# Optimization experiments

Measured on AMD Instinct MI355X. Metric: run time of the kernel, lower is better.

Reference implementation:

```python
import jax, jax.numpy as jnp
import numpy as np

D = 1024
H = 16
HD = D // H
EPS = 1e-5


def layer_norm(x, g, b):
    mu = jnp.mean(x, axis=-1, keepdims=True)
    var = jnp.var(x, axis=-1, keepdims=True)
    return (x - mu) * jax.lax.rsqrt(var + EPS) * g + b


def setup_inputs() -> dict:
    key = jax.random.key(0)
    ks = jax.random.split(key, 16)
    s = 0.02
    return {
        "x": jax.random.normal(ks[0], (2, 2048, D), jnp.float32),
        "ln1_g": jnp.ones((D,), jnp.float32),
        "ln1_b": jnp.zeros((D,), jnp.float32),
        "Wq": jax.random.normal(ks[1], (D, D), jnp.float32) * s,
        "bq": jnp.zeros((D,), jnp.float32),
        "Wk": jax.random.normal(ks[2], (D, D), jnp.float32) * s,
        "bk": jnp.zeros((D,), jnp.float32),
        "Wv": jax.random.normal(ks[3], (D, D), jnp.float32) * s,
        "bv": jnp.zeros((D,), jnp.float32),
        "Wo": jax.random.normal(ks[4], (D, D), jnp.float32) * s,
        "bo": jnp.zeros((D,), jnp.float32),
        "ln2_g": jnp.ones((D,), jnp.float32),
        "ln2_b": jnp.zeros((D,), jnp.float32),
        "W1": jax.random.normal(ks[5], (D, 4 * D), jnp.float32) * s,
        "b1": jnp.zeros((4 * D,), jnp.float32),
        "W2": jax.random.normal(ks[6], (4 * D, D), jnp.float32) * s,
        "b2": jnp.zeros((D,), jnp.float32),
    }


def reference(x, ln1_g, ln1_b, Wq, bq, Wk, bk, Wv, bv, Wo, bo, ln2_g, ln2_b, W1, b1, W2, b2):
    B, T, _ = x.shape
    # --- attention sub-block (pre-LN) ---
    h = layer_norm(x, ln1_g, ln1_b)
    q = (h @ Wq + bq).reshape(B, T, H, HD).transpose(0, 2, 1, 3)  # [B,H,T,hd]
    k = (h @ Wk + bk).reshape(B, T, H, HD).transpose(0, 2, 1, 3)
    v = (h @ Wv + bv).reshape(B, T, H, HD).transpose(0, 2, 1, 3)
    scores = jnp.einsum("bhqd,bhkd->bhqk", q, k)  # full O(T^2) scores as in source
    causal = jnp.tril(jnp.ones((T, T), bool))
    scores = jnp.where(causal, scores, -jnp.inf)
    w = jax.nn.softmax(scores / np.sqrt(HD), axis=-1)
    ctx = jnp.einsum("bhqk,bhkd->bhqd", w, v)
    ctx = ctx.transpose(0, 2, 1, 3).reshape(B, T, D)
    x = x + (ctx @ Wo + bo)
    # --- MLP sub-block (pre-LN) ---
    h = layer_norm(x, ln2_g, ln2_b)
    h = jax.nn.gelu(h @ W1 + b1, approximate=False)
    x = x + (h @ W2 + b2)
    return x
```

## Files before the change

### kernel.cpp

```cpp
#include <hip/hip_runtime.h>
#include <math.h>


typedef _Float16 half8 __attribute__((ext_vector_type(8)));
typedef _Float16 half4v __attribute__((ext_vector_type(4)));
typedef float floatx4 __attribute__((ext_vector_type(4)));

#define DMODEL 1024
#define SEQT   2048
#define NTOK   4096
#define NHEAD  16
#define HDIM   64

__device__ __forceinline__ void llds16(const _Float16* g, _Float16* l) {
  __builtin_amdgcn_global_load_lds(
      (const __attribute__((address_space(1))) void*)g,
      (__attribute__((address_space(3))) void*)l, 16, 0, 0);
}

__global__ __launch_bounds__(256) void wtrans_kernel(
    const float* __restrict__ Wq, const float* __restrict__ Wk,
    const float* __restrict__ Wv, const float* __restrict__ Wo,
    const float* __restrict__ W1, const float* __restrict__ W2,
    _Float16* __restrict__ wt_base) {
  __shared__ float tilebuf[32][33];
  int id = blockIdx.x;
  const float* src; _Float16* dst; int K, N, t;
  if (id < 4096) {
    int s = id >> 10;
    src = (s == 0) ? Wq : (s == 1) ? Wk : (s == 2) ? Wv : Wo;
    dst = wt_base + (size_t)s * (1024 * 1024);
    K = 1024; N = 1024; t = id & 1023;
  } else if (id < 8192) {
    src = W1; dst = wt_base + (size_t)4 * 1024 * 1024; K = 1024; N = 4096; t = id - 4096;
  } else {
    src = W2; dst = wt_base + (size_t)8 * 1024 * 1024; K = 4096; N = 1024; t = id - 8192;
  }
  int tilesN = N >> 5;
  int tk = t / tilesN, tn = t % tilesN;
  int c = threadIdx.x & 31, r0 = threadIdx.x >> 5;
#pragma unroll
  for (int i = 0; i < 4; ++i) {
    int r = r0 + i * 8;
    tilebuf[r][c] = src[(size_t)(tk * 32 + r) * N + tn * 32 + c];
  }
  __syncthreads();
#pragma unroll
  for (int i = 0; i < 4; ++i) {
    int r = r0 + i * 8;
    dst[(size_t)(tn * 32 + r) * K + tk * 32 + c] = (_Float16)tilebuf[c][r];
  }
}

__global__ __launch_bounds__(256) void ln_kernel(
    const float* __restrict__ x, const float* __restrict__ g,
    const float* __restrict__ b, _Float16* __restrict__ out) {
  int row = blockIdx.x;
  int t = threadIdx.x;
  const float4 xv = ((const float4*)(x + (size_t)row * DMODEL))[t];
  float s = xv.x + xv.y + xv.z + xv.w;
  float s2 = xv.x * xv.x + xv.y * xv.y + xv.z * xv.z + xv.w * xv.w;
#pragma unroll
  for (int off = 32; off; off >>= 1) {
    s += __shfl_down(s, off);
    s2 += __shfl_down(s2, off);
  }
  __shared__ float red[8];
  int wid = t >> 6;
  if ((t & 63) == 0) { red[wid] = s; red[wid + 4] = s2; }
  __syncthreads();
  s = red[0] + red[1] + red[2] + red[3];
  s2 = red[4] + red[5] + red[6] + red[7];
  float mu = s * (1.0f / DMODEL);
  float var = s2 * (1.0f / DMODEL) - mu * mu;
  float rstd = rsqrtf(var + 1e-5f);
  const float4 gv = ((const float4*)g)[t];
  const float4 bv = ((const float4*)b)[t];
  half4v o;
  o[0] = (_Float16)((xv.x - mu) * rstd * gv.x + bv.x);
  o[1] = (_Float16)((xv.y - mu) * rstd * gv.y + bv.y);
  o[2] = (_Float16)((xv.z - mu) * rstd * gv.z + bv.z);
  o[3] = (_Float16)((xv.w - mu) * rstd * gv.w + bv.w);
  *(half4v*)(out + (size_t)row * DMODEL + t * 4) = o;
}

template <int MODE>
__global__ __launch_bounds__(256) void gemm_kernel(
    const _Float16* __restrict__ A, const _Float16* __restrict__ Bt0, int K,
    const float* __restrict__ bias0, const float* __restrict__ bias1,
    const float* __restrict__ bias2, const float* __restrict__ res,
    float* __restrict__ outf, _Float16* __restrict__ outh) {
  constexpr int NT = (MODE == 1) ? 64 : 128;
  constexpr int MI = (NT == 128) ? 4 : 2;
  constexpr int BCH = NT / 64;
  __shared__ __align__(16) _Float16 As[2][128 * 32];
  __shared__ __align__(16) _Float16 Bs[2][NT * 32];
  const int tid = threadIdx.x;
  const int m0 = blockIdx.x * 128;
  const _Float16* Bt;
  const float* bias;
  _Float16* outh_sel = outh;
  int n0, sel = 0;
  if (MODE == 0) {
    sel = blockIdx.y >> 3;
    n0 = (blockIdx.y & 7) * 128;
    Bt = Bt0 + (size_t)sel * (1024 * 1024);
    bias = (sel == 0) ? bias0 : (sel == 1) ? bias1 : bias2;
    outh_sel = outh + (size_t)sel * ((size_t)NTOK * DMODEL);
  } else {
    n0 = blockIdx.y * NT;
    Bt = Bt0;
    bias = bias0;
  }
  const int w = tid >> 6, lane = tid & 63;
  const int l15 = lane & 15, q8 = lane >> 4;
  const int wrow = (NT == 128) ? (w >> 1) * 64 : w * 32;
  const int wcol = (NT == 128) ? (w & 1) * 64 : 0;

  const _Float16* gA[2]; int ldsA[2];
  const _Float16* gB[BCH]; int ldsB[BCH];
#pragma unroll
  for (int i = 0; i < 2; ++i) {
    int c0 = i * 256 + w * 64;
    int idx = c0 + lane;
    int m = idx >> 2, kq = (idx & 3) * 8;
    gA[i] = A + (size_t)(m0 + m) * K + kq;
    ldsA[i] = c0 * 8;
  }
#pragma unroll
  for (int i = 0; i < BCH; ++i) {
    int c0 = i * 256 + w * 64;
    int idx = c0 + lane;
    int m = idx >> 2, kq = (idx & 3) * 8;
    gB[i] = Bt + (size_t)(n0 + m) * K + kq;
    ldsB[i] = c0 * 8;
  }

  auto stage = [&](int buf) {
#pragma unroll
    for (int i = 0; i < 2; ++i) {
      llds16(gA[i], &As[buf][ldsA[i]]);
      gA[i] += 32;
    }
#pragma unroll
    for (int i = 0; i < BCH; ++i) {
      llds16(gB[i], &Bs[buf][ldsB[i]]);
      gB[i] += 32;
    }
  };

  floatx4 acc[MI][4];
#pragma unroll
  for (int i = 0; i < MI; ++i)
#pragma unroll
    for (int j = 0; j < 4; ++j) acc[i][j] = (floatx4){0.f, 0.f, 0.f, 0.f};

  const int nk = K >> 5;
  stage(0);
  __syncthreads();
  for (int t = 0; t < nk; ++t) {
    const int buf = t & 1;
    if (t + 1 < nk) stage(buf ^ 1);
    half8 af[MI], bf[4];
#pragma unroll
    for (int i = 0; i < MI; ++i)
      af[i] = *(const half8*)&As[buf][(wrow + i * 16 + l15) * 32 + q8 * 8];
#pragma unroll
    for (int j = 0; j < 4; ++j)
      bf[j] = *(const half8*)&Bs[buf][(wcol + j * 16 + l15) * 32 + q8 * 8];
#pragma unroll
    for (int i = 0; i < MI; ++i)
#pragma unroll
      for (int j = 0; j < 4; ++j)
        acc[i][j] = __builtin_amdgcn_mfma_f32_16x16x32_f16(af[i], bf[j], acc[i][j], 0, 0, 0);
    __syncthreads();
  }

#pragma unroll
  for (int i = 0; i < MI; ++i) {
    int rowb = m0 + wrow + i * 16 + q8 * 4;
#pragma unroll
    for (int j = 0; j < 4; ++j) {
      int col = n0 + wcol + j * 16 + l15;
      float bval = bias[col];
#pragma unroll
      for (int r = 0; r < 4; ++r) {
        int row = rowb + r;
        float v = acc[i][j][r] + bval;
        if (MODE == 0) {
          int bb = row >> 11, tt = row & 2047;
          int hh = col >> 6, hd = col & 63;
          if (sel == 2)
            outh_sel[((size_t)(bb * NHEAD + hh) * HDIM + hd) * SEQT + tt] = (_Float16)v;
          else
            outh_sel[((size_t)(bb * NHEAD + hh) * SEQT + tt) * HDIM + hd] = (_Float16)v;
        } else if (MODE == 1) {
          v += res[(size_t)row * 1024 + col];
          outf[(size_t)row * 1024 + col] = v;
        } else {
          float z = 1.5957691216f * v * (1.0f + 0.044715f * v * v);
          float gl = v / (1.0f + __expf(-z));
          outh[(size_t)row * 4096 + col] = (_Float16)gl;
        }
      }
    }
  }
}

__global__ __launch_bounds__(256) void attn_kernel(
    const _Float16* __restrict__ q, const _Float16* __restrict__ k,
    const _Float16* __restrict__ vt, _Float16* __restrict__ ctx) {
  __shared__ __align__(16) _Float16 Ks[2][64 * 64];
  __shared__ __align__(16) _Float16 Vs[2][64 * 64];
  __shared__ __align__(16) _Float16 Pl[4 * 32 * 72];
  __shared__ float Linv[128];
  const int tid = threadIdx.x;
  const int w = tid >> 6, lane = tid & 63;
  const int l15 = lane & 15, q8 = lane >> 4;
  const int bh = blockIdx.y;
  const int qt0 = blockIdx.x * 128;
  const int qw = qt0 + w * 32;
  const size_t base = (size_t)bh * SEQT * HDIM;

  half8 bq[2][2];
#pragma unroll
  for (int nt = 0; nt < 2; ++nt) {
    const half8* qp = (const half8*)(q + base + (size_t)(qw + nt * 16 + l15) * HDIM);
#pragma unroll
    for (int kc = 0; kc < 2; ++kc) bq[nt][kc] = qp[kc * 4 + q8];
  }

  const _Float16* gk[2]; const _Float16* gv[2]; int ldsc[2];
#pragma unroll
  for (int i = 0; i < 2; ++i) {
    int c0 = i * 256 + w * 64;
    int idx = c0 + lane;
    int r = idx >> 3, c8 = (idx & 7) * 8;
    gk[i] = k + base + (size_t)r * HDIM + c8;
    gv[i] = vt + base + (size_t)r * SEQT + c8;
    ldsc[i] = c0 * 8;
  }
  auto stage = [&](int buf) {
#pragma unroll
    for (int i = 0; i < 2; ++i) {
      llds16(gk[i], &Ks[buf][ldsc[i]]);
      llds16(gv[i], &Vs[buf][ldsc[i]]);
      gk[i] += 64 * HDIM;
      gv[i] += 64;
    }
  };

  floatx4 acc_o[2][4];
#pragma unroll
  for (int i = 0; i < 2; ++i)
#pragma unroll
    for (int j = 0; j < 4; ++j) acc_o[i][j] = (floatx4){0.f, 0.f, 0.f, 0.f};
  float lsum[2] = {0.f, 0.f};
  _Float16* Pw = Pl + w * (32 * 72);

  const int ntiles = 2 * blockIdx.x + 2;
  stage(0);
  __syncthreads();
  for (int jt = 0; jt < ntiles; ++jt) {
    const int buf = jt & 1;
    if (jt + 1 < ntiles) stage(buf ^ 1);

    floatx4 s[4][2];
#pragma unroll
    for (int mt = 0; mt < 4; ++mt)
#pragma unroll
      for (int nt = 0; nt < 2; ++nt) s[mt][nt] = (floatx4){0.f, 0.f, 0.f, 0.f};
#pragma unroll
    for (int mt = 0; mt < 4; ++mt) {
      half8 ak0 = *(const half8*)&Ks[buf][(mt * 16 + l15) * 64 + q8 * 8];
      half8 ak1 = *(const half8*)&Ks[buf][(mt * 16 + l15) * 64 + 32 + q8 * 8];
#pragma unroll
      for (int nt = 0; nt < 2; ++nt) {
        s[mt][nt] = __builtin_amdgcn_mfma_f32_16x16x32_f16(ak0, bq[nt][0], s[mt][nt], 0, 0, 0);
        s[mt][nt] = __builtin_amdgcn_mfma_f32_16x16x32_f16(ak1, bq[nt][1], s[mt][nt], 0, 0, 0);
      }
    }

    const bool masked = (jt >= 2 * (int)blockIdx.x);
#pragma unroll
    for (int mt = 0; mt < 4; ++mt) {
#pragma unroll
      for (int nt = 0; nt < 2; ++nt) {
        half4v ph;
#pragma unroll
        for (int r = 0; r < 4; ++r) {
          float p = __expf(s[mt][nt][r] * 0.125f);
          if (masked) {
            int key = jt * 64 + mt * 16 + q8 * 4 + r;
            int qr = qw + nt * 16 + l15;
            p = (key <= qr) ? p : 0.f;
          }
          lsum[nt] += p;
          ph[r] = (_Float16)p;
        }
        *(half4v*)&Pw[(nt * 16 + l15) * 72 + mt * 16 + q8 * 4] = ph;
      }
    }

#pragma unroll
    for (int kc = 0; kc < 2; ++kc) {
      half8 ap0 = *(const half8*)&Pw[(l15) * 72 + kc * 32 + q8 * 8];
      half8 ap1 = *(const half8*)&Pw[(16 + l15) * 72 + kc * 32 + q8 * 8];
#pragma unroll
      for (int ntd = 0; ntd < 4; ++ntd) {
        half8 bv = *(const half8*)&Vs[buf][(ntd * 16 + l15) * 64 + kc * 32 + q8 * 8];
        acc_o[0][ntd] = __builtin_amdgcn_mfma_f32_16x16x32_f16(ap0, bv, acc_o[0][ntd], 0, 0, 0);
        acc_o[1][ntd] = __builtin_amdgcn_mfma_f32_16x16x32_f16(ap1, bv, acc_o[1][ntd], 0, 0, 0);
      }
    }
    __syncthreads();
  }

#pragma unroll
  for (int nt = 0; nt < 2; ++nt) {
    lsum[nt] += __shfl_xor(lsum[nt], 16);
    lsum[nt] += __shfl_xor(lsum[nt], 32);
    if (q8 == 0) Linv[w * 32 + nt * 16 + l15] = 1.0f / lsum[nt];
  }
  __syncthreads();
  const int b = bh >> 4, h = bh & 15;
#pragma unroll
  for (int mtq = 0; mtq < 2; ++mtq) {
#pragma unroll
    for (int r = 0; r < 4; ++r) {
      int qrl = mtq * 16 + q8 * 4 + r;
      float inv = Linv[w * 32 + qrl];
      int t = qw + qrl;
      _Float16* op = ctx + ((size_t)(b * SEQT + t)) * DMODEL + h * HDIM;
#pragma unroll
      for (int ntd = 0; ntd < 4; ++ntd)
        op[ntd * 16 + l15] = (_Float16)(acc_o[mtq][ntd][r] * inv);
    }
  }
}

extern "C" void kernel_launch(void* const* d_in, const int* in_sizes, int n_in,
                              void* d_out, int out_size, void* d_ws, size_t ws_size,
                              hipStream_t stream) {
  (void)in_sizes; (void)n_in; (void)out_size; (void)ws_size;
  const float* x    = (const float*)d_in[0];
  const float* ln1g = (const float*)d_in[1];
  const float* ln1b = (const float*)d_in[2];
  const float* Wq   = (const float*)d_in[3];
  const float* bq   = (const float*)d_in[4];
  const float* Wk   = (const float*)d_in[5];
  const float* bk   = (const float*)d_in[6];
  const float* Wv   = (const float*)d_in[7];
  const float* bv   = (const float*)d_in[8];
  const float* Wo   = (const float*)d_in[9];
  const float* bo   = (const float*)d_in[10];
  const float* ln2g = (const float*)d_in[11];
  const float* ln2b = (const float*)d_in[12];
  const float* W1   = (const float*)d_in[13];
  const float* b1   = (const float*)d_in[14];
  const float* W2   = (const float*)d_in[15];
  const float* b2   = (const float*)d_in[16];
  float* out = (float*)d_out;

  char* ws = (char*)d_ws;
  _Float16* wt    = (_Float16*)(ws);
  _Float16* h16   = (_Float16*)(ws + ((size_t)24 << 20));
  _Float16* qkv   = (_Float16*)(ws + ((size_t)32 << 20));
  _Float16* ctx16 = (_Float16*)(ws + ((size_t)24 << 20));
  float*    x1    = (float*)   (ws + ((size_t)32 << 20));
  _Float16* h2    = (_Float16*)(ws + ((size_t)48 << 20));
  _Float16* mid   = (_Float16*)(ws + ((size_t)56 << 20));

  const size_t QKV1 = (size_t)NTOK * DMODEL;

  wtrans_kernel<<<12288, 256, 0, stream>>>(Wq, Wk, Wv, Wo, W1, W2, wt);
  ln_kernel<<<NTOK, 256, 0, stream>>>(x, ln1g, ln1b, h16);
  gemm_kernel<0><<<dim3(32, 24), 256, 0, stream>>>(
      h16, wt, 1024, bq, bk, bv, nullptr, nullptr, qkv);
  attn_kernel<<<dim3(SEQT / 128, 32), 256, 0, stream>>>(
      qkv, qkv + QKV1, qkv + 2 * QKV1, ctx16);
  gemm_kernel<1><<<dim3(32, 16), 256, 0, stream>>>(
      ctx16, wt + (size_t)3 * 1024 * 1024, 1024, bo, nullptr, nullptr, x, x1, nullptr);
  ln_kernel<<<NTOK, 256, 0, stream>>>(x1, ln2g, ln2b, h2);
  gemm_kernel<2><<<dim3(32, 32), 256, 0, stream>>>(
      h2, wt + (size_t)4 * 1024 * 1024, 1024, b1, nullptr, nullptr, nullptr, nullptr, mid);
  gemm_kernel<1><<<dim3(32, 16), 256, 0, stream>>>(
      mid, wt + (size_t)8 * 1024 * 1024, 4096, b2, nullptr, nullptr, x1, out, nullptr);
}
```

Baseline: 404.6 us.

## Pair causal query tiles per block and split keys across waves in attention

The attention kernel now handles two 64-row query tiles per block (tiles pr and 31-pr), so every block does the same amount of causal work and one K/V staging pipeline runs across both phases. Within a block the four waves split the 64 keys of each tile rather than the query rows. Partial row sums are combined through shared memory, and an XOR swizzle is applied to the K/V shared-memory layout to reduce bank conflicts. The cost is two block-wide barriers per key tile and a shared P buffer, which may add synchronisation stalls.

```diff
diff --git a/kernel.cpp b/kernel.cpp
--- a/kernel.cpp
+++ b/kernel.cpp
@@ -212,129 +212,115 @@
     const _Float16* __restrict__ vt, _Float16* __restrict__ ctx) {
   __shared__ __align__(16) _Float16 Ks[2][64 * 64];
   __shared__ __align__(16) _Float16 Vs[2][64 * 64];
-  __shared__ __align__(16) _Float16 Pl[4 * 32 * 72];
-  __shared__ float Linv[128];
+  __shared__ __align__(16) _Float16 Ps[64 * 72];
+  __shared__ float Lpart[4][64];
   const int tid = threadIdx.x;
   const int w = tid >> 6, lane = tid & 63;
   const int l15 = lane & 15, q8 = lane >> 4;
   const int bh = blockIdx.y;
-  const int qt0 = blockIdx.x * 128;
-  const int qw = qt0 + w * 32;
+  const int pr = blockIdx.x;
   const size_t base = (size_t)bh * SEQT * HDIM;
 
-  half8 bq[2][2];
-#pragma unroll
-  for (int nt = 0; nt < 2; ++nt) {
-    const half8* qp = (const half8*)(q + base + (size_t)(qw + nt * 16 + l15) * HDIM);
-#pragma unroll
-    for (int kc = 0; kc < 2; ++kc) bq[nt][kc] = qp[kc * 4 + q8];
-  }
-
-  const _Float16* gk[2]; const _Float16* gv[2]; int ldsc[2];
+  const _Float16* gk0[2]; const _Float16* gv0[2]; int ldsc[2];
 #pragma unroll
   for (int i = 0; i < 2; ++i) {
-    int c0 = i * 256 + w * 64;
-    int idx = c0 + lane;
-    int r = idx >> 3, c8 = (idx & 7) * 8;
-    gk[i] = k + base + (size_t)r * HDIM + c8;
-    gv[i] = vt + base + (size_t)r * SEQT + c8;
-    ldsc[i] = c0 * 8;
-  }
-  auto stage = [&](int buf) {
+    int c = i * 256 + w * 64 + lane;
+    int r = c >> 3, gc = ((c & 7) ^ (r & 7)) * 8;
+    gk0[i] = k + base + (size_t)r * HDIM + gc;
+    gv0[i] = vt + base + (size_t)r * SEQT + gc;
+    ldsc[i] = c * 8;
+  }
+  auto stage = [&](int kt, int buf) {
 #pragma unroll
     for (int i = 0; i < 2; ++i) {
-      llds16(gk[i], &Ks[buf][ldsc[i]]);
-      llds16(gv[i], &Vs[buf][ldsc[i]]);
-      gk[i] += 64 * HDIM;
-      gv[i] += 64;
+      llds16(gk0[i] + (size_t)kt * (64 * HDIM), &Ks[buf][ldsc[i]]);
+      llds16(gv0[i] + kt * 64, &Vs[buf][ldsc[i]]);
     }
   };
 
-  floatx4 acc_o[2][4];
-#pragma unroll
-  for (int i = 0; i < 2; ++i)
-#pragma unroll
-    for (int j = 0; j < 4; ++j) acc_o[i][j] = (floatx4){0.f, 0.f, 0.f, 0.f};
-  float lsum[2] = {0.f, 0.f};
-  _Float16* Pw = Pl + w * (32 * 72);
-
-  const int ntiles = 2 * blockIdx.x + 2;
-  stage(0);
+  const int rswA = (l15 & 7);
+  const int cs0 = (q8 ^ rswA) * 8;
+  const int cs1 = ((4 + q8) ^ rswA) * 8;
+
+  int s = 0;
+  stage(0, 0);
   __syncthreads();
-  for (int jt = 0; jt < ntiles; ++jt) {
-    const int buf = jt & 1;
-    if (jt + 1 < ntiles) stage(buf ^ 1);
-
-    floatx4 s[4][2];
-#pragma unroll
-    for (int mt = 0; mt < 4; ++mt)
-#pragma unroll
-      for (int nt = 0; nt < 2; ++nt) s[mt][nt] = (floatx4){0.f, 0.f, 0.f, 0.f};
-#pragma unroll
-    for (int mt = 0; mt < 4; ++mt) {
-      half8 ak0 = *(const half8*)&Ks[buf][(mt * 16 + l15) * 64 + q8 * 8];
-      half8 ak1 = *(const half8*)&Ks[buf][(mt * 16 + l15) * 64 + 32 + q8 * 8];
-#pragma unroll
-      for (int nt = 0; nt < 2; ++nt) {
-        s[mt][nt] = __builtin_amdgcn_mfma_f32_16x16x32_f16(ak0, bq[nt][0], s[mt][nt], 0, 0, 0);
-        s[mt][nt] = __builtin_amdgcn_mfma_f32_16x16x32_f16(ak1, bq[nt][1], s[mt][nt], 0, 0, 0);
-      }
-    }
-
-    const bool masked = (jt >= 2 * (int)blockIdx.x);
-#pragma unroll
-    for (int mt = 0; mt < 4; ++mt) {
-#pragma unroll
-      for (int nt = 0; nt < 2; ++nt) {
-        half4v ph;
+  for (int ph = 0; ph < 2; ++ph) {
+    const int qtile = ph ? 31 - pr : pr;
+    const int ntile = qtile + 1;
+    half8 bq[4][2];
+#pragma unroll
+    for (int nt = 0; nt < 4; ++nt) {
+      const half8* qp = (const half8*)(q + base + (size_t)(qtile * 64 + nt * 16 + l15) * HDIM);
+      bq[nt][0] = qp[q8];
+      bq[nt][1] = qp[4 + q8];
+    }
+    floatx4 acc[4];
+#pragma unroll
+    for (int j = 0; j < 4; ++j) acc[j] = (floatx4){0.f, 0.f, 0.f, 0.f};
+    float lsum[4] = {0.f, 0.f, 0.f, 0.f};
+
+    for (int jt = 0; jt < ntile; ++jt, ++s) {
+      const int buf = s & 1;
+      if (s + 1 < 33) {
+        int sn = s + 1;
+        int nkt = (sn <= pr) ? sn : sn - (pr + 1);
+        stage(nkt, buf ^ 1);
+      }
+      half8 ak0 = *(const half8*)&Ks[buf][(w * 16 + l15) * 64 + cs0];
+      half8 ak1 = *(const half8*)&Ks[buf][(w * 16 + l15) * 64 + cs1];
+      floatx4 sv[4];
+#pragma unroll
+      for (int nt = 0; nt < 4; ++nt) {
+        sv[nt] = __builtin_amdgcn_mfma_f32_16x16x32_f16(ak0, bq[nt][0],
+                                                        (floatx4){0.f, 0.f, 0.f, 0.f}, 0, 0, 0);
+        sv[nt] = __builtin_amdgcn_mfma_f32_16x16x32_f16(ak1, bq[nt][1], sv[nt], 0, 0, 0);
+      }
+      const bool diag = (jt == ntile - 1);
+#pragma unroll
+      for (int nt = 0; nt < 4; ++nt) {
+        half4v phv;
 #pragma unroll
         for (int r = 0; r < 4; ++r) {
-          float p = __expf(s[mt][nt][r] * 0.125f);
-          if (masked) {
-            int key = jt * 64 + mt * 16 + q8 * 4 + r;
-            int qr = qw + nt * 16 + l15;
-            p = (key <= qr) ? p : 0.f;
+          float p = __expf(sv[nt][r] * 0.125f);
+          if (diag) {
+            p = (w * 16 + q8 * 4 + r <= nt * 16 + l15) ? p : 0.f;
           }
           lsum[nt] += p;
-          ph[r] = (_Float16)p;
+          phv[r] = (_Float16)p;
         }
-        *(half4v*)&Pw[(nt * 16 + l15) * 72 + mt * 16 + q8 * 4] = ph;
-      }
-    }
-
-#pragma unroll
-    for (int kc = 0; kc < 2; ++kc) {
-      half8 ap0 = *(const half8*)&Pw[(l15) * 72 + kc * 32 + q8 * 8];
-      half8 ap1 = *(const half8*)&Pw[(16 + l15) * 72 + kc * 32 + q8 * 8];
+        *(half4v*)&Ps[(nt * 16 + l15) * 72 + w * 16 + q8 * 4] = phv;
+      }
+      __syncthreads();
+      half8 ap0 = *(const half8*)&Ps[(w * 16 + l15) * 72 + q8 * 8];
+      half8 ap1 = *(const half8*)&Ps[(w * 16 + l15) * 72 + 32 + q8 * 8];
 #pragma unroll
       for (int ntd = 0; ntd < 4; ++ntd) {
-        half8 bv = *(const half8*)&Vs[buf][(ntd * 16 + l15) * 64 + kc * 32 + q8 * 8];
-        acc_o[0][ntd] = __builtin_amdgcn_mfma_f32_16x16x32_f16(ap0, bv, acc_o[0][ntd], 0, 0, 0);
-        acc_o[1][ntd] = __builtin_amdgcn_mfma_f32_16x16x32_f16(ap1, bv, acc_o[1][ntd], 0, 0, 0);
-      }
+        half8 bv0 = *(const half8*)&Vs[buf][(ntd * 16 + l15) * 64 + cs0];
+        half8 bv1 = *(const half8*)&Vs[buf][(ntd * 16 + l15) * 64 + cs1];
+        acc[ntd] = __builtin_amdgcn_mfma_f32_16x16x32_f16(ap0, bv0, acc[ntd], 0, 0, 0);
+        acc[ntd] = __builtin_amdgcn_mfma_f32_16x16x32_f16(ap1, bv1, acc[ntd], 0, 0, 0);
+      }
+      __syncthreads();
+    }
+
+#pragma unroll
+    for (int nt = 0; nt < 4; ++nt) {
+      lsum[nt] += __shfl_xor(lsum[nt], 16);
+      lsum[nt] += __shfl_xor(lsum[nt], 32);
+      if (q8 == 0) Lpart[w][nt * 16 + l15] = lsum[nt];
     }
     __syncthreads();
-  }
-
-#pragma unroll
-  for (int nt = 0; nt < 2; ++nt) {
-    lsum[nt] += __shfl_xor(lsum[nt], 16);
-    lsum[nt] += __shfl_xor(lsum[nt], 32);
-    if (q8 == 0) Linv[w * 32 + nt * 16 + l15] = 1.0f / lsum[nt];
-  }
-  __syncthreads();
-  const int b = bh >> 4, h = bh & 15;
-#pragma unroll
-  for (int mtq = 0; mtq < 2; ++mtq) {
+    const int b = bh >> 4, h = bh & 15;
 #pragma unroll
     for (int r = 0; r < 4; ++r) {
-      int qrl = mtq * 16 + q8 * 4 + r;
-      float inv = Linv[w * 32 + qrl];
-      int t = qw + qrl;
-      _Float16* op = ctx + ((size_t)(b * SEQT + t)) * DMODEL + h * HDIM;
+      int qr = w * 16 + q8 * 4 + r;
+      float inv = 1.0f / (Lpart[0][qr] + Lpart[1][qr] + Lpart[2][qr] + Lpart[3][qr]);
+      int tg = qtile * 64 + qr;
+      _Float16* op = ctx + ((size_t)(b * SEQT + tg)) * DMODEL + h * HDIM;
 #pragma unroll
       for (int ntd = 0; ntd < 4; ++ntd)
-        op[ntd * 16 + l15] = (_Float16)(acc_o[mtq][ntd][r] * inv);
+        op[ntd * 16 + l15] = (_Float16)(acc[ntd][r] * inv);
     }
   }
 }
@@ -377,7 +363,7 @@
   ln_kernel<<<NTOK, 256, 0, stream>>>(x, ln1g, ln1b, h16);
   gemm_kernel<0><<<dim3(32, 24), 256, 0, stream>>>(
       h16, wt, 1024, bq, bk, bv, nullptr, nullptr, qkv);
-  attn_kernel<<<dim3(SEQT / 128, 32), 256, 0, stream>>>(
+  attn_kernel<<<dim3(16, 32), 256, 0, stream>>>(
       qkv, qkv + QKV1, qkv + 2 * QKV1, ctx16);
   gemm_kernel<1><<<dim3(32, 16), 256, 0, stream>>>(
       ctx16, wt + (size_t)3 * 1024 * 1024, 1024, bo, nullptr, nullptr, x, x1, nullptr);
```

Measured after the change: 379.5 us. 6.2% less time.
